# Kernel optimization log

Hardware: AMD Instinct MI355X
Metric: run time of the kernel (lower is better)

Reference implementation:

```python
import jax, jax.numpy as jnp
import numpy as np


def _conv1x1(x, w, b):
    # x: [B,C,H,W], w: [O,C], b: [O] -> [B,O,H,W]
    return jnp.einsum('oc,bchw->bohw', w, x) + b[None, :, None, None]


def setup_inputs() -> dict:
    key = jax.random.key(0)
    ks = jax.random.split(key, 9)
    B, C, O, H, W = 8, 192, 96, 64, 64
    s_in = 1.0 / np.sqrt(C)
    s_out = 1.0 / np.sqrt(O)
    return {
        'x': jax.random.normal(ks[0], (B, C, H, W), dtype=jnp.float32),
        'g_w': jax.random.normal(ks[1], (O, C), dtype=jnp.float32) * s_in,
        'g_b': jax.random.normal(ks[2], (O,), dtype=jnp.float32) * s_in,
        'theta_w': jax.random.normal(ks[3], (O, C), dtype=jnp.float32) * s_in,
        'theta_b': jax.random.normal(ks[4], (O,), dtype=jnp.float32) * s_in,
        'phi_w': jax.random.normal(ks[5], (O, C), dtype=jnp.float32) * s_in,
        'phi_b': jax.random.normal(ks[6], (O,), dtype=jnp.float32) * s_in,
        'W_w': jax.random.normal(ks[7], (C, O), dtype=jnp.float32) * s_out,
        'W_b': jax.random.normal(ks[8], (C,), dtype=jnp.float32) * s_out,
    }


def reference(x, g_w, g_b, theta_w, theta_b, phi_w, phi_b, W_w, W_b):
    B, C, H, W = x.shape
    O = g_w.shape[0]
    N = H * W
    # 1x1 conv projections, flattened to [B, O, N]
    g_x = _conv1x1(x, g_w, g_b).reshape(B, O, N)          # [B,O,N]
    theta_x = _conv1x1(x, theta_w, theta_b).reshape(B, O, N)
    phi_x = _conv1x1(x, phi_w, phi_b).reshape(B, O, N)
    # scores f1[b,n,m] = theta[:, :, n] . phi[:, :, m]
    f1 = jnp.einsum('bon,bom->bnm', theta_x, phi_x)       # [B,N,N]
    f_div_C = jax.nn.softmax(f1, axis=-1)
    # y[b,n,o] = sum_m f[b,n,m] * g[b,o,m]
    y = jnp.einsum('bnm,bom->bon', f_div_C, g_x)          # [B,O,N]
    y = y.reshape(B, O, H, W)
    W_y = _conv1x1(y, W_w, W_b)                           # [B,C,H,W]
    return W_y + x
```

## Files before the change

### kernel.cpp

```cpp
#include <hip/hip_runtime.h>

typedef unsigned short u16;
typedef unsigned int u32;
typedef float f32x4 __attribute__((ext_vector_type(4)));
typedef float f32x16 __attribute__((ext_vector_type(16)));
typedef _Float16 h16x8 __attribute__((ext_vector_type(8)));
typedef u32 u32x4 __attribute__((ext_vector_type(4)));
typedef u32 u32x2 __attribute__((ext_vector_type(2)));
typedef u16 u16x4 __attribute__((ext_vector_type(4)));

#define NB 8
#define CC 192
#define OO 96
#define NN 4096
#define NSPLIT 3
#define XPAD 200

static __device__ __forceinline__ u16 f2h(float f) {
  _Float16 h = (_Float16)f;
  return __builtin_bit_cast(u16, h);
}
static __device__ __forceinline__ float h2f(u16 u) {
  return (float)__builtin_bit_cast(_Float16, u);
}
static __device__ __forceinline__ void gl_lds16(const u16* g, u16* l) {
  __builtin_amdgcn_global_load_lds(
      (const __attribute__((address_space(1))) void*)g,
      (__attribute__((address_space(3))) void*)l, 16, 0, 0);
}
static __device__ __forceinline__ void plane_swap(u32& a, u32& b) {
  u32x2 r = __builtin_amdgcn_permlane32_swap(a, b, false, false);
  a = r[0]; b = r[1];
}
static __device__ __forceinline__ float half_combine_max(float x) {
  u32 a = __builtin_bit_cast(u32, x), b = a;
  plane_swap(a, b);
  return fmaxf(__builtin_bit_cast(float, a), __builtin_bit_cast(float, b));
}
static __device__ __forceinline__ float half_combine_sum(float x) {
  u32 a = __builtin_bit_cast(u32, x), b = a;
  plane_swap(a, b);
  return __builtin_bit_cast(float, a) + __builtin_bit_cast(float, b);
}

__global__ __launch_bounds__(256) void proj_kernel(
    const float* __restrict__ x,
    const float* __restrict__ g_w, const float* __restrict__ g_b,
    const float* __restrict__ th_w, const float* __restrict__ th_b,
    const float* __restrict__ ph_w, const float* __restrict__ ph_b,
    u16* __restrict__ QB, u16* __restrict__ KA, u16* __restrict__ VA)
{
  __shared__ __align__(16) u16 Xs[64][XPAD];
  __shared__ __align__(16) u16 Ws[96][XPAD];
  const int b = blockIdx.y, n0 = blockIdx.x * 64, tid = threadIdx.x;
  const int lane = tid & 63, wv = tid >> 6, l15 = lane & 15, lg = lane >> 4;

  #pragma unroll
  for (int it = 0; it < 12; ++it) {
    int idx = tid + it * 256;
    int c = idx >> 4, q = idx & 15;
    float4 v = *(const float4*)(x + ((size_t)(b * CC + c)) * NN + n0 + q * 4);
    Xs[q * 4 + 0][c] = f2h(v.x); Xs[q * 4 + 1][c] = f2h(v.y);
    Xs[q * 4 + 2][c] = f2h(v.z); Xs[q * 4 + 3][c] = f2h(v.w);
  }

  for (int p = 0; p < 3; ++p) {
    const float* w    = (p == 0) ? th_w : (p == 1) ? ph_w : g_w;
    const float* bias = (p == 0) ? th_b : (p == 1) ? ph_b : g_b;
    __syncthreads();
    #pragma unroll
    for (int it = 0; it < 18; ++it) {
      int idx = tid + it * 256;
      int r = idx / 48, q = idx % 48;
      float4 v = *(const float4*)(w + r * CC + q * 4);
      u16x4 hh; hh[0] = f2h(v.x); hh[1] = f2h(v.y); hh[2] = f2h(v.z); hh[3] = f2h(v.w);
      *(u16x4*)&Ws[r][q * 4] = hh;
    }
    __syncthreads();

    f32x4 acc[6];
    #pragma unroll
    for (int of = 0; of < 6; ++of) acc[of] = (f32x4){0.f, 0.f, 0.f, 0.f};
    #pragma unroll
    for (int ks = 0; ks < 6; ++ks) {
      h16x8 xa = *(const h16x8*)&Xs[wv * 16 + l15][ks * 32 + lg * 8];
      #pragma unroll
      for (int of = 0; of < 6; ++of) {
        h16x8 wf = *(const h16x8*)&Ws[of * 16 + l15][ks * 32 + lg * 8];
        if (p < 2) acc[of] = __builtin_amdgcn_mfma_f32_16x16x32_f16(xa, wf, acc[of], 0, 0, 0);
        else       acc[of] = __builtin_amdgcn_mfma_f32_16x16x32_f16(wf, xa, acc[of], 0, 0, 0);
      }
    }

    if (p < 2) {
      u16* dst = (p == 0) ? QB : KA;
      #pragma unroll
      for (int of = 0; of < 6; ++of) {
        int o = of * 16 + l15;
        float bo = bias[o];
        int kch = of * 2 + (l15 >> 3);
        #pragma unroll
        for (int r = 0; r < 4; ++r) {
          int n = n0 + wv * 16 + lg * 4 + r;
          int idx = (b * 128 + (n >> 5)) * 3072 + (kch * 32 + (n & 31)) * 8 + (o & 7);
          dst[idx] = f2h(acc[of][r] + bo);
        }
      }
    } else {
      #pragma unroll
      for (int of = 0; of < 6; ++of) {
        #pragma unroll
        for (int r = 0; r < 4; ++r) {
          int o = of * 16 + lg * 4 + r;
          int m = n0 + wv * 16 + l15;
          int idx = (b * 256 + (m >> 4)) * 1536 +
                    (((o >> 5) * 2 + ((m >> 3) & 1)) * 32 + (o & 31)) * 8 + (m & 7);
          VA[idx] = f2h(acc[of][r] + bias[o]);
        }
      }
    }
  }
}

__global__ __launch_bounds__(256, 3) void attn_kernel(
    const u16* __restrict__ QB, const u16* __restrict__ KA,
    const u16* __restrict__ VA, u16* __restrict__ yP, float* __restrict__ ml)
{
  __shared__ __align__(16) u16 Ks[2][6144];
  __shared__ __align__(16) u16 Vs[2][6144];
  const int b   = blockIdx.x;
  const int qt  = blockIdx.y;
  const int sp  = blockIdx.z;
  const int tid = threadIdx.x;
  const int lane = tid & 63;
  const int wv  = tid >> 6;
  const int l31 = lane & 31;
  const int h   = lane >> 5;

  const int t_start = (64 * sp) / NSPLIT;
  const int t_end   = (64 * (sp + 1)) / NSPLIT;
  const int nt = t_end - t_start;

  const int nc = qt * 4 + wv;
  const u16* qb = QB + (size_t)(b * 128 + nc) * 3072;
  h16x8 qf[6];
  #pragma unroll
  for (int ks = 0; ks < 6; ++ks)
    qf[ks] = *(const h16x8*)(qb + ((ks * 2 + h) * 32 + l31) * 8);

  const u16* KAb = KA + (size_t)b * (128 * 3072);
  const u16* VAb = VA + (size_t)b * (256 * 1536);

  f32x16 acc[3];
  #pragma unroll
  for (int ob = 0; ob < 3; ++ob)
    #pragma unroll
    for (int i = 0; i < 16; ++i) acc[ob][i] = 0.f;
  float m_run = -__builtin_inff(), l_run = 0.f;

  {
    const u16* gk = KAb + (size_t)t_start * 6144;
    const u16* gv = VAb + (size_t)t_start * 6144;
    #pragma unroll
    for (int i = 0; i < 3; ++i) gl_lds16(gk + tid * 8 + i * 2048, &Ks[0][tid * 8 + i * 2048]);
    #pragma unroll
    for (int i = 0; i < 3; ++i) gl_lds16(gv + tid * 8 + i * 2048, &Vs[0][tid * 8 + i * 2048]);
  }

  for (int t = 0; t < nt; ++t) {
    const int bf = t & 1;
    if (t + 1 < nt) {
      const u16* gk = KAb + (size_t)(t_start + t + 1) * 6144;
      const u16* gv = VAb + (size_t)(t_start + t + 1) * 6144;
      #pragma unroll
      for (int i = 0; i < 3; ++i) gl_lds16(gk + tid * 8 + i * 2048, &Ks[bf ^ 1][tid * 8 + i * 2048]);
      #pragma unroll
      for (int i = 0; i < 3; ++i) gl_lds16(gv + tid * 8 + i * 2048, &Vs[bf ^ 1][tid * 8 + i * 2048]);
      asm volatile("s_waitcnt vmcnt(6)" ::: "memory");
    } else {
      asm volatile("s_waitcnt vmcnt(0)" ::: "memory");
    }
    __builtin_amdgcn_s_barrier();
    __builtin_amdgcn_sched_barrier(0);

    #pragma unroll
    for (int c = 0; c < 2; ++c) {
      f32x16 S;
      #pragma unroll
      for (int i = 0; i < 16; ++i) S[i] = 0.f;
      const u16* kbase = &Ks[bf][c * 3072];
      #pragma unroll
      for (int ks = 0; ks < 6; ++ks) {
        h16x8 kf = *(const h16x8*)(kbase + ((ks * 2 + h) * 32 + l31) * 8);
        S = __builtin_amdgcn_mfma_f32_32x32x16_f16(kf, qf[ks], S, 0, 0, 0);
      }
      float v[16];
      #pragma unroll
      for (int i = 0; i < 16; ++i) v[i] = S[i];
      #pragma unroll
      for (int st = 8; st >= 1; st >>= 1)
        #pragma unroll
        for (int i = 0; i < 8; ++i) if (i < st) v[i] = fmaxf(v[i], v[i + st]);
      float pmax = half_combine_max(v[0]);
      if (__ballot(pmax > m_run + 8.0f)) {
        float mn = fmaxf(m_run, pmax);
        float sc = __expf(m_run - mn);
        m_run = mn; l_run *= sc;
        #pragma unroll
        for (int ob = 0; ob < 3; ++ob)
          #pragma unroll
          for (int i = 0; i < 16; ++i) acc[ob][i] *= sc;
      }
      float p[16];
      #pragma unroll
      for (int i = 0; i < 16; ++i) p[i] = __expf(S[i] - m_run);
      #pragma unroll
      for (int i = 0; i < 16; ++i) v[i] = p[i];
      #pragma unroll
      for (int st = 8; st >= 1; st >>= 1)
        #pragma unroll
        for (int i = 0; i < 8; ++i) if (i < st) v[i] += v[i + st];
      l_run += half_combine_sum(v[0]);
      u32 pk[8];
      #pragma unroll
      for (int i = 0; i < 8; ++i)
        pk[i] = __builtin_bit_cast(u32, __builtin_amdgcn_cvt_pkrtz(p[2 * i], p[2 * i + 1]));
      plane_swap(pk[0], pk[2]); plane_swap(pk[1], pk[3]);
      plane_swap(pk[4], pk[6]); plane_swap(pk[5], pk[7]);
      u32x4 bw0 = {pk[0], pk[1], pk[2], pk[3]};
      u32x4 bw1 = {pk[4], pk[5], pk[6], pk[7]};
      h16x8 pf0 = __builtin_bit_cast(h16x8, bw0);
      h16x8 pf1 = __builtin_bit_cast(h16x8, bw1);
      const u16* vbase = &Vs[bf][c * 3072];
      #pragma unroll
      for (int s2 = 0; s2 < 2; ++s2) {
        h16x8 pfr = s2 ? pf1 : pf0;
        #pragma unroll
        for (int ob = 0; ob < 3; ++ob) {
          h16x8 vf = *(const h16x8*)(vbase + (((s2 * 3 + ob) * 2 + h) * 32 + l31) * 8);
          acc[ob] = __builtin_amdgcn_mfma_f32_32x32x16_f16(vf, pfr, acc[ob], 0, 0, 0);
        }
      }
    }
    __builtin_amdgcn_s_barrier();
    __builtin_amdgcn_sched_barrier(0);
  }

  float inv = 1.0f / l_run;
  int nglob = nc * 32 + l31;
  u16* yp = yP + (((size_t)sp * NB + b) * NN + nglob) * OO;
  #pragma unroll
  for (int ob = 0; ob < 3; ++ob) {
    #pragma unroll
    for (int rq = 0; rq < 4; ++rq) {
      int o0 = ob * 32 + rq * 8 + h * 4;
      u32 w0 = __builtin_bit_cast(u32,
          __builtin_amdgcn_cvt_pkrtz(acc[ob][rq * 4 + 0] * inv, acc[ob][rq * 4 + 1] * inv));
      u32 w1 = __builtin_bit_cast(u32,
          __builtin_amdgcn_cvt_pkrtz(acc[ob][rq * 4 + 2] * inv, acc[ob][rq * 4 + 3] * inv));
      uint2 pr; pr.x = w0; pr.y = w1;
      *(uint2*)&yp[o0] = pr;
    }
  }
  if (h == 0) {
    float2 v2; v2.x = m_run; v2.y = l_run;
    *(float2*)&ml[(((size_t)sp * NB + b) * NN + nglob) * 2] = v2;
  }
}

__global__ __launch_bounds__(256) void merge_kernel(
    const u16* __restrict__ yP, const float* __restrict__ ml, u16* __restrict__ yT16)
{
  size_t t = (size_t)blockIdx.x * 256 + threadIdx.x;
  int o = (int)(t % OO);
  size_t bn = t / OO;
  const size_t SB = (size_t)NB * NN;
  float m0 = ml[(0 * SB + bn) * 2], l0 = ml[(0 * SB + bn) * 2 + 1];
  float m1 = ml[(1 * SB + bn) * 2], l1 = ml[(1 * SB + bn) * 2 + 1];
  float m2 = ml[(2 * SB + bn) * 2], l2 = ml[(2 * SB + bn) * 2 + 1];
  float M = fmaxf(m0, fmaxf(m1, m2));
  float w0 = l0 * __expf(m0 - M), w1 = l1 * __expf(m1 - M), w2 = l2 * __expf(m2 - M);
  float y0 = h2f(yP[(0 * SB + bn) * OO + o]);
  float y1 = h2f(yP[(1 * SB + bn) * OO + o]);
  float y2 = h2f(yP[(2 * SB + bn) * OO + o]);
  float y = (w0 * y0 + w1 * y1 + w2 * y2) / (w0 + w1 + w2);
  yT16[bn * OO + o] = f2h(y);
}

#define YPAD 104
__global__ __launch_bounds__(256) void outproj_kernel(
    const float* __restrict__ x, const float* __restrict__ Ww,
    const float* __restrict__ Wb, const u16* __restrict__ yT16,
    float* __restrict__ out)
{
  __shared__ __align__(16) u16 Wws[CC][YPAD];
  __shared__ __align__(16) u16 Ys[64][YPAD];
  const int b = blockIdx.y, n0 = blockIdx.x * 64, tid = threadIdx.x;
  const int lane = tid & 63, wv = tid >> 6, l15 = lane & 15, lg = lane >> 4;

  #pragma unroll
  for (int it = 0; it < 18; ++it) {
    int idx = tid + it * 256;
    int r = idx / 24, q = idx % 24;
    float4 v = *(const float4*)(Ww + r * OO + q * 4);
    u16x4 hh; hh[0] = f2h(v.x); hh[1] = f2h(v.y); hh[2] = f2h(v.z); hh[3] = f2h(v.w);
    *(u16x4*)&Wws[r][q * 4] = hh;
  }
  #pragma unroll
  for (int it = 0; it < 3; ++it) {
    int idx = tid + it * 256;
    int n = idx / 12, q = idx % 12;
    *(float4*)&Ys[n][q * 8] =
        *(const float4*)(yT16 + ((size_t)(b * NN + n0 + n)) * OO + q * 8);
  }
  __syncthreads();

  f32x4 acc[12];
  #pragma unroll
  for (int cf = 0; cf < 12; ++cf) acc[cf] = (f32x4){0.f, 0.f, 0.f, 0.f};
  #pragma unroll
  for (int ks = 0; ks < 3; ++ks) {
    h16x8 yb = *(const h16x8*)&Ys[wv * 16 + l15][ks * 32 + lg * 8];
    #pragma unroll
    for (int cf = 0; cf < 12; ++cf) {
      h16x8 wa = *(const h16x8*)&Wws[cf * 16 + l15][ks * 32 + lg * 8];
      acc[cf] = __builtin_amdgcn_mfma_f32_16x16x32_f16(wa, yb, acc[cf], 0, 0, 0);
    }
  }
  #pragma unroll
  for (int cf = 0; cf < 12; ++cf) {
    #pragma unroll
    for (int r = 0; r < 4; ++r) {
      int c = cf * 16 + lg * 4 + r;
      size_t off = ((size_t)(b * CC + c)) * NN + n0 + wv * 16 + l15;
      out[off] = acc[cf][r] + x[off] + Wb[c];
    }
  }
}

extern "C" void kernel_launch(void* const* d_in, const int* in_sizes, int n_in,
                              void* d_out, int out_size, void* d_ws, size_t ws_size,
                              hipStream_t stream) {
  const float* x    = (const float*)d_in[0];
  const float* g_w  = (const float*)d_in[1];
  const float* g_b  = (const float*)d_in[2];
  const float* th_w = (const float*)d_in[3];
  const float* th_b = (const float*)d_in[4];
  const float* ph_w = (const float*)d_in[5];
  const float* ph_b = (const float*)d_in[6];
  const float* W_w  = (const float*)d_in[7];
  const float* W_b  = (const float*)d_in[8];
  float* out = (float*)d_out;

  char* ws = (char*)d_ws;
  const size_t projB = (size_t)NB * NN * OO * sizeof(u16);
  u16* QB   = (u16*)ws;
  u16* KA   = (u16*)(ws + projB);
  u16* VA   = (u16*)(ws + 2 * projB);
  u16* yP   = (u16*)(ws + 3 * projB);
  float* ml = (float*)(ws + 6 * projB);
  u16* yT16 = QB;

  dim3 blk(256);
  dim3 gproj(64, NB);
  hipLaunchKernelGGL(proj_kernel, gproj, blk, 0, stream,
                     x, g_w, g_b, th_w, th_b, ph_w, ph_b, QB, KA, VA);
  dim3 gattn(NB, 32, NSPLIT);
  hipLaunchKernelGGL(attn_kernel, gattn, blk, 0, stream, QB, KA, VA, yP, ml);
  dim3 gmerge((NB * NN * OO) / 256);
  hipLaunchKernelGGL(merge_kernel, gmerge, blk, 0, stream, yP, ml, yT16);
  dim3 gout(64, NB);
  hipLaunchKernelGGL(outproj_kernel, gout, blk, 0, stream, x, W_w, W_b, yT16, out);
}
```

Measured before the change: 106.7 us.

## Fuse split-merge into outproj, use exp2 softmax, process two key chunks together

The separate merge kernel is removed, and the outproj kernel now combines the three split partial outputs using the m/l statistics while loading Y tiles. This saves one launch and an intermediate round trip through global memory. The theta projection is pre-scaled by log2(e) so the attention softmax can use exp2f directly, with the lazy-rescale threshold adjusted to match. The attention inner loop now computes both 32-key score chunks together with one max/rescale per tile and interleaved MFMAs, and uses setprio around the MFMA blocks. This raises register pressure.

```diff
diff --git a/kernel.cpp b/kernel.cpp
--- a/kernel.cpp
+++ b/kernel.cpp
@@ -15,13 +15,11 @@
 #define NN 4096
 #define NSPLIT 3
 #define XPAD 200
+#define LOG2E 1.4426950408889634f
 
 static __device__ __forceinline__ u16 f2h(float f) {
   _Float16 h = (_Float16)f;
   return __builtin_bit_cast(u16, h);
-}
-static __device__ __forceinline__ float h2f(u16 u) {
-  return (float)__builtin_bit_cast(_Float16, u);
 }
 static __device__ __forceinline__ void gl_lds16(const u16* g, u16* l) {
   __builtin_amdgcn_global_load_lds(
@@ -41,6 +39,9 @@
   u32 a = __builtin_bit_cast(u32, x), b = a;
   plane_swap(a, b);
   return __builtin_bit_cast(float, a) + __builtin_bit_cast(float, b);
+}
+static __device__ __forceinline__ float max3f(float a, float b, float c) {
+  return fmaxf(fmaxf(a, b), c);
 }
 
 __global__ __launch_bounds__(256) void proj_kernel(
@@ -67,13 +68,15 @@
   for (int p = 0; p < 3; ++p) {
     const float* w    = (p == 0) ? th_w : (p == 1) ? ph_w : g_w;
     const float* bias = (p == 0) ? th_b : (p == 1) ? ph_b : g_b;
+    const float scale = (p == 0) ? LOG2E : 1.0f;
     __syncthreads();
     #pragma unroll
     for (int it = 0; it < 18; ++it) {
       int idx = tid + it * 256;
       int r = idx / 48, q = idx % 48;
       float4 v = *(const float4*)(w + r * CC + q * 4);
-      u16x4 hh; hh[0] = f2h(v.x); hh[1] = f2h(v.y); hh[2] = f2h(v.z); hh[3] = f2h(v.w);
+      u16x4 hh; hh[0] = f2h(v.x * scale); hh[1] = f2h(v.y * scale);
+      hh[2] = f2h(v.z * scale); hh[3] = f2h(v.w * scale);
       *(u16x4*)&Ws[r][q * 4] = hh;
     }
     __syncthreads();
@@ -97,7 +100,7 @@
       #pragma unroll
       for (int of = 0; of < 6; ++of) {
         int o = of * 16 + l15;
-        float bo = bias[o];
+        float bo = bias[o] * scale;
         int kch = of * 2 + (l15 >> 3);
         #pragma unroll
         for (int r = 0; r < 4; ++r) {
@@ -156,7 +159,7 @@
   for (int ob = 0; ob < 3; ++ob)
     #pragma unroll
     for (int i = 0; i < 16; ++i) acc[ob][i] = 0.f;
-  float m_run = -__builtin_inff(), l_run = 0.f;
+  float m_run = -3.0e38f, l_run = 0.f;
 
   {
     const u16* gk = KAb + (size_t)t_start * 6144;
@@ -183,65 +186,77 @@
     __builtin_amdgcn_s_barrier();
     __builtin_amdgcn_sched_barrier(0);
 
-    #pragma unroll
-    for (int c = 0; c < 2; ++c) {
-      f32x16 S;
-      #pragma unroll
-      for (int i = 0; i < 16; ++i) S[i] = 0.f;
-      const u16* kbase = &Ks[bf][c * 3072];
-      #pragma unroll
-      for (int ks = 0; ks < 6; ++ks) {
-        h16x8 kf = *(const h16x8*)(kbase + ((ks * 2 + h) * 32 + l31) * 8);
-        S = __builtin_amdgcn_mfma_f32_32x32x16_f16(kf, qf[ks], S, 0, 0, 0);
+    f32x16 S0, S1;
+    #pragma unroll
+    for (int i = 0; i < 16; ++i) { S0[i] = 0.f; S1[i] = 0.f; }
+    const u16* kb0 = &Ks[bf][0];
+    const u16* kb1 = &Ks[bf][3072];
+    __builtin_amdgcn_s_setprio(1);
+    #pragma unroll
+    for (int ks = 0; ks < 6; ++ks) {
+      h16x8 kf0 = *(const h16x8*)(kb0 + ((ks * 2 + h) * 32 + l31) * 8);
+      S0 = __builtin_amdgcn_mfma_f32_32x32x16_f16(kf0, qf[ks], S0, 0, 0, 0);
+      h16x8 kf1 = *(const h16x8*)(kb1 + ((ks * 2 + h) * 32 + l31) * 8);
+      S1 = __builtin_amdgcn_mfma_f32_32x32x16_f16(kf1, qf[ks], S1, 0, 0, 0);
+    }
+    __builtin_amdgcn_s_setprio(0);
+
+    float v[16];
+    #pragma unroll
+    for (int i = 0; i < 16; ++i) v[i] = fmaxf(S0[i], S1[i]);
+    float t0 = max3f(v[0], v[1], v[2]),  t1 = max3f(v[3], v[4], v[5]);
+    float t2 = max3f(v[6], v[7], v[8]),  t3 = max3f(v[9], v[10], v[11]);
+    float t4 = max3f(v[12], v[13], v[14]);
+    float pmax = half_combine_max(fmaxf(max3f(t0, t1, t2), max3f(t3, t4, v[15])));
+    if (__ballot(pmax > m_run + 11.5416f)) {
+      float mn = fmaxf(m_run, pmax);
+      float sc = exp2f(m_run - mn);
+      m_run = mn; l_run *= sc;
+      #pragma unroll
+      for (int ob = 0; ob < 3; ++ob)
+        #pragma unroll
+        for (int i = 0; i < 16; ++i) acc[ob][i] *= sc;
+    }
+    float p0[16], p1[16];
+    #pragma unroll
+    for (int i = 0; i < 16; ++i) { p0[i] = exp2f(S0[i] - m_run); p1[i] = exp2f(S1[i] - m_run); }
+    #pragma unroll
+    for (int i = 0; i < 16; ++i) v[i] = p0[i] + p1[i];
+    #pragma unroll
+    for (int st = 8; st >= 1; st >>= 1)
+      #pragma unroll
+      for (int i = 0; i < 8; ++i) if (i < st) v[i] += v[i + st];
+    l_run += half_combine_sum(v[0]);
+
+    u32 pk0[8], pk1[8];
+    #pragma unroll
+    for (int i = 0; i < 8; ++i) {
+      pk0[i] = __builtin_bit_cast(u32, __builtin_amdgcn_cvt_pkrtz(p0[2 * i], p0[2 * i + 1]));
+      pk1[i] = __builtin_bit_cast(u32, __builtin_amdgcn_cvt_pkrtz(p1[2 * i], p1[2 * i + 1]));
+    }
+    plane_swap(pk0[0], pk0[2]); plane_swap(pk0[1], pk0[3]);
+    plane_swap(pk0[4], pk0[6]); plane_swap(pk0[5], pk0[7]);
+    plane_swap(pk1[0], pk1[2]); plane_swap(pk1[1], pk1[3]);
+    plane_swap(pk1[4], pk1[6]); plane_swap(pk1[5], pk1[7]);
+    u32x4 c00 = {pk0[0], pk0[1], pk0[2], pk0[3]}, c01 = {pk0[4], pk0[5], pk0[6], pk0[7]};
+    u32x4 c10 = {pk1[0], pk1[1], pk1[2], pk1[3]}, c11 = {pk1[4], pk1[5], pk1[6], pk1[7]};
+    h16x8 pf[4] = {__builtin_bit_cast(h16x8, c00), __builtin_bit_cast(h16x8, c01),
+                   __builtin_bit_cast(h16x8, c10), __builtin_bit_cast(h16x8, c11)};
+
+    const u16* vb0 = &Vs[bf][0];
+    const u16* vb1 = &Vs[bf][3072];
+    __builtin_amdgcn_s_setprio(1);
+    #pragma unroll
+    for (int s2 = 0; s2 < 2; ++s2) {
+      #pragma unroll
+      for (int ob = 0; ob < 3; ++ob) {
+        h16x8 vf0 = *(const h16x8*)(vb0 + (((s2 * 3 + ob) * 2 + h) * 32 + l31) * 8);
+        acc[ob] = __builtin_amdgcn_mfma_f32_32x32x16_f16(vf0, pf[s2], acc[ob], 0, 0, 0);
+        h16x8 vf1 = *(const h16x8*)(vb1 + (((s2 * 3 + ob) * 2 + h) * 32 + l31) * 8);
+        acc[ob] = __builtin_amdgcn_mfma_f32_32x32x16_f16(vf1, pf[2 + s2], acc[ob], 0, 0, 0);
       }
-      float v[16];
-      #pragma unroll
-      for (int i = 0; i < 16; ++i) v[i] = S[i];
-      #pragma unroll
-      for (int st = 8; st >= 1; st >>= 1)
-        #pragma unroll
-        for (int i = 0; i < 8; ++i) if (i < st) v[i] = fmaxf(v[i], v[i + st]);
-      float pmax = half_combine_max(v[0]);
-      if (__ballot(pmax > m_run + 8.0f)) {
-        float mn = fmaxf(m_run, pmax);
-        float sc = __expf(m_run - mn);
-        m_run = mn; l_run *= sc;
-        #pragma unroll
-        for (int ob = 0; ob < 3; ++ob)
-          #pragma unroll
-          for (int i = 0; i < 16; ++i) acc[ob][i] *= sc;
-      }
-      float p[16];
-      #pragma unroll
-      for (int i = 0; i < 16; ++i) p[i] = __expf(S[i] - m_run);
-      #pragma unroll
-      for (int i = 0; i < 16; ++i) v[i] = p[i];
-      #pragma unroll
-      for (int st = 8; st >= 1; st >>= 1)
-        #pragma unroll
-        for (int i = 0; i < 8; ++i) if (i < st) v[i] += v[i + st];
-      l_run += half_combine_sum(v[0]);
-      u32 pk[8];
-      #pragma unroll
-      for (int i = 0; i < 8; ++i)
-        pk[i] = __builtin_bit_cast(u32, __builtin_amdgcn_cvt_pkrtz(p[2 * i], p[2 * i + 1]));
-      plane_swap(pk[0], pk[2]); plane_swap(pk[1], pk[3]);
-      plane_swap(pk[4], pk[6]); plane_swap(pk[5], pk[7]);
-      u32x4 bw0 = {pk[0], pk[1], pk[2], pk[3]};
-      u32x4 bw1 = {pk[4], pk[5], pk[6], pk[7]};
-      h16x8 pf0 = __builtin_bit_cast(h16x8, bw0);
-      h16x8 pf1 = __builtin_bit_cast(h16x8, bw1);
-      const u16* vbase = &Vs[bf][c * 3072];
-      #pragma unroll
-      for (int s2 = 0; s2 < 2; ++s2) {
-        h16x8 pfr = s2 ? pf1 : pf0;
-        #pragma unroll
-        for (int ob = 0; ob < 3; ++ob) {
-          h16x8 vf = *(const h16x8*)(vbase + (((s2 * 3 + ob) * 2 + h) * 32 + l31) * 8);
-          acc[ob] = __builtin_amdgcn_mfma_f32_32x32x16_f16(vf, pfr, acc[ob], 0, 0, 0);
-        }
-      }
-    }
+    }
+    __builtin_amdgcn_s_setprio(0);
     __builtin_amdgcn_s_barrier();
     __builtin_amdgcn_sched_barrier(0);
   }
@@ -268,35 +283,17 @@
   }
 }
 
-__global__ __launch_bounds__(256) void merge_kernel(
-    const u16* __restrict__ yP, const float* __restrict__ ml, u16* __restrict__ yT16)
-{
-  size_t t = (size_t)blockIdx.x * 256 + threadIdx.x;
-  int o = (int)(t % OO);
-  size_t bn = t / OO;
-  const size_t SB = (size_t)NB * NN;
-  float m0 = ml[(0 * SB + bn) * 2], l0 = ml[(0 * SB + bn) * 2 + 1];
-  float m1 = ml[(1 * SB + bn) * 2], l1 = ml[(1 * SB + bn) * 2 + 1];
-  float m2 = ml[(2 * SB + bn) * 2], l2 = ml[(2 * SB + bn) * 2 + 1];
-  float M = fmaxf(m0, fmaxf(m1, m2));
-  float w0 = l0 * __expf(m0 - M), w1 = l1 * __expf(m1 - M), w2 = l2 * __expf(m2 - M);
-  float y0 = h2f(yP[(0 * SB + bn) * OO + o]);
-  float y1 = h2f(yP[(1 * SB + bn) * OO + o]);
-  float y2 = h2f(yP[(2 * SB + bn) * OO + o]);
-  float y = (w0 * y0 + w1 * y1 + w2 * y2) / (w0 + w1 + w2);
-  yT16[bn * OO + o] = f2h(y);
-}
-
 #define YPAD 104
 __global__ __launch_bounds__(256) void outproj_kernel(
     const float* __restrict__ x, const float* __restrict__ Ww,
-    const float* __restrict__ Wb, const u16* __restrict__ yT16,
-    float* __restrict__ out)
+    const float* __restrict__ Wb, const u16* __restrict__ yP,
+    const float* __restrict__ ml, float* __restrict__ out)
 {
   __shared__ __align__(16) u16 Wws[CC][YPAD];
   __shared__ __align__(16) u16 Ys[64][YPAD];
   const int b = blockIdx.y, n0 = blockIdx.x * 64, tid = threadIdx.x;
   const int lane = tid & 63, wv = tid >> 6, l15 = lane & 15, lg = lane >> 4;
+  const size_t SB = (size_t)NB * NN;
 
   #pragma unroll
   for (int it = 0; it < 18; ++it) {
@@ -310,8 +307,25 @@
   for (int it = 0; it < 3; ++it) {
     int idx = tid + it * 256;
     int n = idx / 12, q = idx % 12;
-    *(float4*)&Ys[n][q * 8] =
-        *(const float4*)(yT16 + ((size_t)(b * NN + n0 + n)) * OO + q * 8);
+    size_t bn = (size_t)b * NN + n0 + n;
+    float m0 = ml[(0 * SB + bn) * 2], l0 = ml[(0 * SB + bn) * 2 + 1];
+    float m1 = ml[(1 * SB + bn) * 2], l1 = ml[(1 * SB + bn) * 2 + 1];
+    float m2 = ml[(2 * SB + bn) * 2], l2 = ml[(2 * SB + bn) * 2 + 1];
+    float M = max3f(m0, m1, m2);
+    float w0 = l0 * exp2f(m0 - M), w1 = l1 * exp2f(m1 - M), w2 = l2 * exp2f(m2 - M);
+    float rinv = 1.0f / (w0 + w1 + w2);
+    w0 *= rinv; w1 *= rinv; w2 *= rinv;
+    h16x8 y0 = *(const h16x8*)(yP + (0 * SB + bn) * OO + q * 8);
+    h16x8 y1 = *(const h16x8*)(yP + (1 * SB + bn) * OO + q * 8);
+    h16x8 y2 = *(const h16x8*)(yP + (2 * SB + bn) * OO + q * 8);
+    u32x4 packed;
+    #pragma unroll
+    for (int e = 0; e < 4; ++e) {
+      float a = w0 * (float)y0[2 * e]     + w1 * (float)y1[2 * e]     + w2 * (float)y2[2 * e];
+      float c = w0 * (float)y0[2 * e + 1] + w1 * (float)y1[2 * e + 1] + w2 * (float)y2[2 * e + 1];
+      packed[e] = __builtin_bit_cast(u32, __builtin_amdgcn_cvt_pkrtz(a, c));
+    }
+    *(u32x4*)&Ys[n][q * 8] = packed;
   }
   __syncthreads();
 
@@ -359,7 +373,6 @@
   u16* VA   = (u16*)(ws + 2 * projB);
   u16* yP   = (u16*)(ws + 3 * projB);
   float* ml = (float*)(ws + 6 * projB);
-  u16* yT16 = QB;
 
   dim3 blk(256);
   dim3 gproj(64, NB);
@@ -367,8 +380,6 @@
                      x, g_w, g_b, th_w, th_b, ph_w, ph_b, QB, KA, VA);
   dim3 gattn(NB, 32, NSPLIT);
   hipLaunchKernelGGL(attn_kernel, gattn, blk, 0, stream, QB, KA, VA, yP, ml);
-  dim3 gmerge((NB * NN * OO) / 256);
-  hipLaunchKernelGGL(merge_kernel, gmerge, blk, 0, stream, yP, ml, yT16);
   dim3 gout(64, NB);
-  hipLaunchKernelGGL(outproj_kernel, gout, blk, 0, stream, x, W_w, W_b, yT16, out);
-}
+  hipLaunchKernelGGL(outproj_kernel, gout, blk, 0, stream, x, W_w, W_b, yP, ml, out);
+}
```

Result: slower. 110.6 us (+3.6%).
